# Optimization experiments

Measured on AMD Instinct MI355X. Metric: run time of the kernel, lower is better.

## Reference

```python
import jax, jax.numpy as jnp
import numpy as np

EPS = 1e-5  # torch GroupNorm default eps


def gn(x, g, b):
    # GroupNorm with 1 group on [N, C]: normalize over channel dim per row
    mu = jnp.mean(x, axis=-1, keepdims=True)
    var = jnp.var(x, axis=-1, keepdims=True)
    return (x - mu) * jax.lax.rsqrt(var + EPS) * g + b


def setup_inputs() -> dict:
    N, A, E, D = 500000, 20000, 500000, 128
    key = jax.random.key(0)
    ks = jax.random.split(key, 12)
    s = 0.05
    return {
        "map_x": jax.random.normal(ks[0], (N, 8), jnp.float32),
        "agt_x": jax.random.normal(ks[1], (A, 80), jnp.float32),
        "u": jax.random.randint(ks[2], (E,), 0, A),
        "v": jax.random.randint(ks[3], (E,), 0, N),
        # map_fc: Linear(8,D) with bias, then custom Linear(D,D,bias=False)+GN+ReLU
        "W0": jax.random.normal(ks[4], (D, 8), jnp.float32) * s,
        "b0": jnp.zeros((D,), jnp.float32),
        "W1": jax.random.normal(ks[5], (D, D), jnp.float32) * s,
        "g1": jnp.ones((D,), jnp.float32),
        "b1": jnp.zeros((D,), jnp.float32),
        # agt_fc: Linear(80, D, bias=False)
        "Wa": jax.random.normal(ks[6], (D, 80), jnp.float32) * s,
        # self.bn GroupNorm params
        "g_bn": jnp.ones((D,), jnp.float32),
        "b_bn": jnp.zeros((D,), jnp.float32),
        # self.fc: Linear(2D, D, bias=False)+GN+ReLU
        "Wf": jax.random.normal(ks[7], (D, 2 * D), jnp.float32) * s,
        "g_fc": jnp.ones((D,), jnp.float32),
        "b_fc": jnp.zeros((D,), jnp.float32),
    }


def reference(map_x, agt_x, u, v, W0, b0, W1, g1, b1, Wa, g_bn, b_bn, Wf, g_fc, b_fc):
    # map_fc: Linear+ReLU, then Linear(no bias)+GN+ReLU
    h = jax.nn.relu(map_x @ W0.T + b0)                      # [N, D]
    h = jax.nn.relu(gn(h @ W1.T, g1, b1))                   # [N, D]
    # agent messages: project agents once (A < E), then gather per edge
    msg = (agt_x @ Wa.T)[u]                                 # [E, D]
    tmp = jnp.zeros_like(h).at[v].add(msg)                  # scatter-add into map nodes
    tmp = jax.nn.relu(gn(tmp, g_bn, b_bn))                  # [N, D]
    cat = jnp.concatenate([h, tmp], axis=-1)                # [N, 2D]
    out = jax.nn.relu(gn(cat @ Wf.T, g_fc, b_fc))           # [N, D]
    return out
```

## Files before the change

### kernel.cpp

```cpp
#include <hip/hip_runtime.h>
#include <stdint.h>

#define EPS 1e-5f

typedef short bh8 __attribute__((ext_vector_type(8)));
typedef float f4v __attribute__((ext_vector_type(4)));
typedef unsigned short ushort_t;

static __device__ __forceinline__ unsigned short f2bf(float f) {
    unsigned u = __builtin_bit_cast(unsigned, f);
    u += 0x7fffu + ((u >> 16) & 1u);
    return (unsigned short)(u >> 16);
}

static __device__ __forceinline__ float bfbits(unsigned x) {
    return __builtin_bit_cast(float, x);
}

static __device__ __forceinline__ void acc16(float* tv, uint4 qa, uint4 qb) {
    unsigned wd[8] = {qa.x, qa.y, qa.z, qa.w, qb.x, qb.y, qb.z, qb.w};
#pragma unroll
    for (int p = 0; p < 8; ++p) {
        tv[2 * p + 0] += bfbits(wd[p] << 16);
        tv[2 * p + 1] += bfbits(wd[p] & 0xffff0000u);
    }
}


__global__ __launch_bounds__(256) void prep(const float* __restrict__ W1,
                                            const float* __restrict__ Wf,
                                            ushort_t* __restrict__ W1b,
                                            ushort_t* __restrict__ Wfb,
                                            int* __restrict__ cnt, int n) {
    int i = blockIdx.x * 256 + threadIdx.x;
    if (i < 16384) W1b[i] = f2bf(W1[i]);
    else if (i < 49152) { int j = i - 16384; Wfb[j] = f2bf(Wf[j]); }
    for (int k = i; k < n; k += gridDim.x * 256) cnt[k] = 0;
}

__global__ __launch_bounds__(256) void proj_agents(const float* __restrict__ agt,
                                                   const float* __restrict__ Wa,
                                                   unsigned short* __restrict__ Pb) {
    __shared__ float WT[80 * 128];
    __shared__ float xT[80][32];
    int t = threadIdx.x;
    int row0 = blockIdx.x * 32;
#pragma unroll
    for (int m = 0; m < 40; ++m) {
        int f = t + 256 * m;
        int k = f >> 7, c = f & 127;
        WT[f] = Wa[c * 80 + k];
    }
#pragma unroll
    for (int m = 0; m < 10; ++m) {
        int f = t + 256 * m;
        int r = f / 80, k = f - r * 80;
        xT[k][r] = agt[(size_t)(row0 + r) * 80 + k];
    }
    __syncthreads();
    int tx = t & 31, ty = t >> 5;
    float acc[4][4] = {};
    for (int k = 0; k < 80; ++k) {
        float4 xv = *(const float4*)&xT[k][ty * 4];
        float4 wv = *(const float4*)&WT[k * 128 + tx * 4];
        float xa[4] = {xv.x, xv.y, xv.z, xv.w};
        float wa[4] = {wv.x, wv.y, wv.z, wv.w};
#pragma unroll
        for (int i = 0; i < 4; ++i)
#pragma unroll
            for (int j = 0; j < 4; ++j) acc[i][j] = fmaf(xa[i], wa[j], acc[i][j]);
    }
#pragma unroll
    for (int i = 0; i < 4; ++i) {
        int r = row0 + ty * 4 + i;
        union { unsigned short s[4]; uint2 q; } o;
#pragma unroll
        for (int j = 0; j < 4; ++j) o.s[j] = f2bf(acc[i][j]);
        *(uint2*)&Pb[(size_t)r * 128 + tx * 4] = o.q;
    }
}

__global__ void hist_v(const int* __restrict__ v, int* __restrict__ cnt, int E) {
    int e = blockIdx.x * 256 + threadIdx.x;
    if (e < E) atomicAdd(&cnt[v[e]], 1);
}

__global__ __launch_bounds__(256) void scan1(const int* __restrict__ cnt,
                                             int* __restrict__ rp,
                                             int* __restrict__ partials, int n) {
    __shared__ int lds[256];
    int b = blockIdx.x, t = threadIdx.x;
    int base = b * 4096 + t * 16;
    int vv[16];
    int run = 0;
#pragma unroll
    for (int i = 0; i < 16; ++i) {
        int c = (base + i < n) ? cnt[base + i] : 0;
        vv[i] = run;
        run += c;
    }
    lds[t] = run;
    __syncthreads();
#pragma unroll
    for (int off = 1; off < 256; off <<= 1) {
        int x = (t >= off) ? lds[t - off] : 0;
        __syncthreads();
        lds[t] += x;
        __syncthreads();
    }
    int excl = lds[t] - run;
    if (t == 255) partials[b] = lds[255];
#pragma unroll
    for (int i = 0; i < 16; ++i)
        if (base + i < n) rp[base + i] = excl + vv[i];
}

__global__ __launch_bounds__(256) void scan2(int* __restrict__ partials, int nb) {
    __shared__ int lds[256];
    int t = threadIdx.x;
    int vv = (t < nb) ? partials[t] : 0;
    lds[t] = vv;
    __syncthreads();
#pragma unroll
    for (int off = 1; off < 256; off <<= 1) {
        int x = (t >= off) ? lds[t - off] : 0;
        __syncthreads();
        lds[t] += x;
        __syncthreads();
    }
    if (t < nb) partials[t] = lds[t] - vv;
}

__global__ void scan3(int* __restrict__ rp, const int* __restrict__ partials,
                      int n, int E) {
    int i = blockIdx.x * 256 + threadIdx.x;
    if (i < n) rp[i] += partials[i >> 12];
    if (i == 0) rp[n] = E;
}

__global__ void fill_csr(const int* __restrict__ u, const int* __restrict__ v,
                         const int* __restrict__ rp, int* __restrict__ cnt,
                         int* __restrict__ col, int E) {
    int e = blockIdx.x * 256 + threadIdx.x;
    if (e < E) {
        int vv = v[e];
        int pos = rp[vv] + (atomicSub(&cnt[vv], 1) - 1);
        col[pos] = u[e];
    }
}

__global__ __launch_bounds__(256) void gather_gn(
    const unsigned short* __restrict__ Pb, const int* __restrict__ rp,
    const int* __restrict__ col, const float* __restrict__ g_bn,
    const float* __restrict__ b_bn, ushort_t* __restrict__ catB) {
    const int t = threadIdx.x;
    const int node = blockIdx.x * 32 + (t >> 3);
    const int c0 = (t & 7) * 16;
    const int beg = rp[node];
    const int deg = rp[node + 1] - beg;
    const int ca = col[(deg > 0) ? beg : 0];
    const int cb = col[(deg > 1) ? beg + 1 : 0];
    const int cc = col[(deg > 2) ? beg + 2 : 0];
    const int cd = col[(deg > 3) ? beg + 3 : 0];
    const unsigned short* pB = Pb + c0;
    float tv[16] = {};
    if (deg > 0) { const uint4* p = (const uint4*)(pB + (size_t)ca * 128); acc16(tv, p[0], p[1]); }
    if (deg > 1) { const uint4* p = (const uint4*)(pB + (size_t)cb * 128); acc16(tv, p[0], p[1]); }
    if (deg > 2) { const uint4* p = (const uint4*)(pB + (size_t)cc * 128); acc16(tv, p[0], p[1]); }
    if (deg > 3) { const uint4* p = (const uint4*)(pB + (size_t)cd * 128); acc16(tv, p[0], p[1]); }
    for (int k = 4; k < deg; ++k) {
        const uint4* p = (const uint4*)(pB + (size_t)col[beg + k] * 128);
        acc16(tv, p[0], p[1]);
    }
    float a = 0.f, q = 0.f;
#pragma unroll
    for (int i = 0; i < 16; ++i) { a += tv[i]; q += tv[i] * tv[i]; }
#pragma unroll
    for (int msk = 1; msk < 8; msk <<= 1) {
        a += __shfl_xor(a, msk, 64);
        q += __shfl_xor(q, msk, 64);
    }
    const float mean = a * (1.f / 128.f);
    const float var = q * (1.f / 128.f) - mean * mean;
    const float inv = rsqrtf(var + EPS);
    union { unsigned short s[16]; uint4 q4[2]; } o;
#pragma unroll
    for (int i = 0; i < 16; ++i) {
        const int cch = c0 + i;
        o.s[i] = f2bf(fmaxf((tv[i] - mean) * inv * g_bn[cch] + b_bn[cch], 0.f));
    }
    uint4* dst = (uint4*)(catB + (size_t)node * 128 + c0);
    dst[0] = o.q4[0];
    dst[1] = o.q4[1];
}

__global__ __launch_bounds__(512, 4) void fused(
    const float* __restrict__ mapx, const float* __restrict__ W0,
    const float* __restrict__ b0, const ushort_t* __restrict__ W1b,
    const float* __restrict__ g1, const float* __restrict__ b1,
    const ushort_t* __restrict__ catB, const ushort_t* __restrict__ Wfb,
    const float* __restrict__ g_fc, const float* __restrict__ b_fc,
    float* __restrict__ out, int ntiles)
{
    __shared__ __align__(16) short h0sA[32 * 128], h0sB[32 * 128];
    __shared__ __align__(16) short catsA[32 * 256], catsB[32 * 256];
    __shared__ float W0s[128 * 8];
    __shared__ float b0s[128];
    __shared__ float2 partA[8][32], partB[8][32];
    __shared__ float gA[128], bA[128], gC[128], bC[128];

    const int t = threadIdx.x;
    const int w = t >> 6;
    const int l = t & 63;
    const int l15 = l & 15, lg = l >> 4;

    if (t < 128) {
        gA[t] = g1[t];   bA[t] = b1[t];
        gC[t] = g_fc[t]; bC[t] = b_fc[t];
        b0s[t] = b0[t];
    }
    for (int i = t; i < 1024; i += 512) W0s[i] = W0[i];

    bh8 w1b[4], wfb[8];
    {
        const int wr = 16 * w + l15;
#pragma unroll
        for (int s = 0; s < 4; ++s)
            w1b[s] = *(const bh8*)(W1b + (size_t)wr * 128 + s * 32 + lg * 8);
#pragma unroll
        for (int s = 0; s < 8; ++s)
            wfb[s] = *(const bh8*)(Wfb + (size_t)wr * 256 + s * 32 + lg * 8);
    }
    __syncthreads();

    const f4v fzero = {0.f, 0.f, 0.f, 0.f};
    const int stride = (int)gridDim.x;
    const int npairs = (ntiles + 1) >> 1;

    for (int j = blockIdx.x; j < npairs; j += stride) {
        const int tileA = 2 * j, tileB = 2 * j + 1;
        const bool hasB = (tileB < ntiles);
        const int rowA0 = tileA * 32, rowB0 = tileB * 32;

        {
            const int r = t & 31, cg = t >> 5;
            const int ad = (r * 256 + cg * 16) ^ ((r & 7) << 4);
            {
                float mx[8];
                const float* p = mapx + (size_t)(rowA0 + r) * 8;
                *(float4*)&mx[0] = *(const float4*)p;
                *(float4*)&mx[4] = *(const float4*)(p + 4);
                __align__(16) unsigned short hb[8];
#pragma unroll
                for (int c = 0; c < 8; ++c) {
                    const int cc = 8 * cg + c;
                    float a = b0s[cc];
#pragma unroll
                    for (int jj = 0; jj < 8; ++jj) a = fmaf(mx[jj], W0s[cc * 8 + jj], a);
                    hb[c] = f2bf(fmaxf(a, 0.f));
                }
                *(uint4*)((char*)h0sA + ad) = *(const uint4*)&hb[0];
            }
            if (hasB) {
                float mx[8];
                const float* p = mapx + (size_t)(rowB0 + r) * 8;
                *(float4*)&mx[0] = *(const float4*)p;
                *(float4*)&mx[4] = *(const float4*)(p + 4);
                __align__(16) unsigned short hb[8];
#pragma unroll
                for (int c = 0; c < 8; ++c) {
                    const int cc = 8 * cg + c;
                    float a = b0s[cc];
#pragma unroll
                    for (int jj = 0; jj < 8; ++jj) a = fmaf(mx[jj], W0s[cc * 8 + jj], a);
                    hb[c] = f2bf(fmaxf(a, 0.f));
                }
                *(uint4*)((char*)h0sB + ad) = *(const uint4*)&hb[0];
            }
        }
        {
            const int r2 = t >> 4, cb = (t & 15) * 8;
            const int ad = (r2 * 512 + 256 + cb * 2) ^ ((r2 & 7) << 4);
            uint4 qa = *(const uint4*)(catB + (size_t)(rowA0 + r2) * 128 + cb);
            *(uint4*)((char*)catsA + ad) = qa;
            if (hasB) {
                uint4 qb = *(const uint4*)(catB + (size_t)(rowB0 + r2) * 128 + cb);
                *(uint4*)((char*)catsB + ad) = qb;
            }
        }
        __syncthreads();

        f4v a2A[2], a2B[2];
        a2A[0] = fzero; a2A[1] = fzero; a2B[0] = fzero; a2B[1] = fzero;
#pragma unroll
        for (int s = 0; s < 4; ++s) {
            bh8 afA[2], afB[2];
#pragma unroll
            for (int m = 0; m < 2; ++m) {
                const int row = 16 * m + l15;
                const int a = (row * 256 + s * 64 + lg * 16) ^ ((row & 7) << 4);
                afA[m] = *(const bh8*)((const char*)h0sA + a);
                afB[m] = *(const bh8*)((const char*)h0sB + a);
            }
#pragma unroll
            for (int m = 0; m < 2; ++m) {
                a2A[m] = __builtin_amdgcn_mfma_f32_16x16x32_bf16(w1b[s], afA[m], a2A[m], 0, 0, 0);
                a2B[m] = __builtin_amdgcn_mfma_f32_16x16x32_bf16(w1b[s], afB[m], a2B[m], 0, 0, 0);
            }
        }

#pragma unroll
        for (int m = 0; m < 2; ++m) {
            float aA = a2A[m][0] + a2A[m][1] + a2A[m][2] + a2A[m][3];
            float qA = a2A[m][0] * a2A[m][0] + a2A[m][1] * a2A[m][1] +
                       a2A[m][2] * a2A[m][2] + a2A[m][3] * a2A[m][3];
            float aB = a2B[m][0] + a2B[m][1] + a2B[m][2] + a2B[m][3];
            float qB = a2B[m][0] * a2B[m][0] + a2B[m][1] * a2B[m][1] +
                       a2B[m][2] * a2B[m][2] + a2B[m][3] * a2B[m][3];
            aA += __shfl_xor(aA, 16, 64); qA += __shfl_xor(qA, 16, 64);
            aA += __shfl_xor(aA, 32, 64); qA += __shfl_xor(qA, 32, 64);
            aB += __shfl_xor(aB, 16, 64); qB += __shfl_xor(qB, 16, 64);
            aB += __shfl_xor(aB, 32, 64); qB += __shfl_xor(qB, 32, 64);
            if (lg == 0) {
                partA[w][16 * m + l15] = make_float2(aA, qA);
                partB[w][16 * m + l15] = make_float2(aB, qB);
            }
        }
        __syncthreads();

#pragma unroll
        for (int m = 0; m < 2; ++m) {
            const int row = 16 * m + l15;
            const int c00 = 16 * w + 4 * lg;
            const int ad = (row * 512 + c00 * 2) ^ ((row & 7) << 4);
            {
                float a = 0.f, q = 0.f;
#pragma unroll
                for (int pw = 0; pw < 8; ++pw) {
                    float2 pq = partA[pw][row];
                    a += pq.x; q += pq.y;
                }
                const float mean = a * (1.f / 128.f);
                const float var = q * (1.f / 128.f) - mean * mean;
                const float inv = rsqrtf(var + EPS);
                union { unsigned short s[4]; uint2 q2; } o;
#pragma unroll
                for (int reg = 0; reg < 4; ++reg) {
                    float v2 = (a2A[m][reg] - mean) * inv * gA[c00 + reg] + bA[c00 + reg];
                    o.s[reg] = f2bf(fmaxf(v2, 0.f));
                }
                *(uint2*)((char*)catsA + ad) = o.q2;
            }
            {
                float a = 0.f, q = 0.f;
#pragma unroll
                for (int pw = 0; pw < 8; ++pw) {
                    float2 pq = partB[pw][row];
                    a += pq.x; q += pq.y;
                }
                const float mean = a * (1.f / 128.f);
                const float var = q * (1.f / 128.f) - mean * mean;
                const float inv = rsqrtf(var + EPS);
                union { unsigned short s[4]; uint2 q2; } o;
#pragma unroll
                for (int reg = 0; reg < 4; ++reg) {
                    float v2 = (a2B[m][reg] - mean) * inv * gA[c00 + reg] + bA[c00 + reg];
                    o.s[reg] = f2bf(fmaxf(v2, 0.f));
                }
                *(uint2*)((char*)catsB + ad) = o.q2;
            }
        }
        __syncthreads();

        f4v a3A[2], a3B[2];
        a3A[0] = fzero; a3A[1] = fzero; a3B[0] = fzero; a3B[1] = fzero;
#pragma unroll
        for (int s = 0; s < 8; ++s) {
            bh8 afA[2], afB[2];
#pragma unroll
            for (int m = 0; m < 2; ++m) {
                const int row = 16 * m + l15;
                const int a = (row * 512 + s * 64 + lg * 16) ^ ((row & 7) << 4);
                afA[m] = *(const bh8*)((const char*)catsA + a);
                afB[m] = *(const bh8*)((const char*)catsB + a);
            }
#pragma unroll
            for (int m = 0; m < 2; ++m) {
                a3A[m] = __builtin_amdgcn_mfma_f32_16x16x32_bf16(wfb[s], afA[m], a3A[m], 0, 0, 0);
                a3B[m] = __builtin_amdgcn_mfma_f32_16x16x32_bf16(wfb[s], afB[m], a3B[m], 0, 0, 0);
            }
        }

#pragma unroll
        for (int m = 0; m < 2; ++m) {
            float aA = a3A[m][0] + a3A[m][1] + a3A[m][2] + a3A[m][3];
            float qA = a3A[m][0] * a3A[m][0] + a3A[m][1] * a3A[m][1] +
                       a3A[m][2] * a3A[m][2] + a3A[m][3] * a3A[m][3];
            float aB = a3B[m][0] + a3B[m][1] + a3B[m][2] + a3B[m][3];
            float qB = a3B[m][0] * a3B[m][0] + a3B[m][1] * a3B[m][1] +
                       a3B[m][2] * a3B[m][2] + a3B[m][3] * a3B[m][3];
            aA += __shfl_xor(aA, 16, 64); qA += __shfl_xor(qA, 16, 64);
            aA += __shfl_xor(aA, 32, 64); qA += __shfl_xor(qA, 32, 64);
            aB += __shfl_xor(aB, 16, 64); qB += __shfl_xor(qB, 16, 64);
            aB += __shfl_xor(aB, 32, 64); qB += __shfl_xor(qB, 32, 64);
            if (lg == 0) {
                partA[w][16 * m + l15] = make_float2(aA, qA);
                partB[w][16 * m + l15] = make_float2(aB, qB);
            }
        }
        __syncthreads();

#pragma unroll
        for (int m = 0; m < 2; ++m) {
            const int row = 16 * m + l15;
            const int c00 = 16 * w + 4 * lg;
            {
                float a = 0.f, q = 0.f;
#pragma unroll
                for (int pw = 0; pw < 8; ++pw) {
                    float2 pq = partA[pw][row];
                    a += pq.x; q += pq.y;
                }
                const float mean = a * (1.f / 128.f);
                const float var = q * (1.f / 128.f) - mean * mean;
                const float inv = rsqrtf(var + EPS);
                float4 o;
                o.x = fmaxf((a3A[m][0] - mean) * inv * gC[c00 + 0] + bC[c00 + 0], 0.f);
                o.y = fmaxf((a3A[m][1] - mean) * inv * gC[c00 + 1] + bC[c00 + 1], 0.f);
                o.z = fmaxf((a3A[m][2] - mean) * inv * gC[c00 + 2] + bC[c00 + 2], 0.f);
                o.w = fmaxf((a3A[m][3] - mean) * inv * gC[c00 + 3] + bC[c00 + 3], 0.f);
                *(float4*)&out[(size_t)(rowA0 + row) * 128 + c00] = o;
            }
            if (hasB) {
                float a = 0.f, q = 0.f;
#pragma unroll
                for (int pw = 0; pw < 8; ++pw) {
                    float2 pq = partB[pw][row];
                    a += pq.x; q += pq.y;
                }
                const float mean = a * (1.f / 128.f);
                const float var = q * (1.f / 128.f) - mean * mean;
                const float inv = rsqrtf(var + EPS);
                float4 o;
                o.x = fmaxf((a3B[m][0] - mean) * inv * gC[c00 + 0] + bC[c00 + 0], 0.f);
                o.y = fmaxf((a3B[m][1] - mean) * inv * gC[c00 + 1] + bC[c00 + 1], 0.f);
                o.z = fmaxf((a3B[m][2] - mean) * inv * gC[c00 + 2] + bC[c00 + 2], 0.f);
                o.w = fmaxf((a3B[m][3] - mean) * inv * gC[c00 + 3] + bC[c00 + 3], 0.f);
                *(float4*)&out[(size_t)(rowB0 + row) * 128 + c00] = o;
            }
        }
    }
}

extern "C" void kernel_launch(void* const* d_in, const int* in_sizes, int n_in,
                              void* d_out, int out_size, void* d_ws, size_t ws_size,
                              hipStream_t stream) {
    const float* mapx = (const float*)d_in[0];
    const float* agt  = (const float*)d_in[1];
    const int*   u    = (const int*)d_in[2];
    const int*   v    = (const int*)d_in[3];
    const float* W0   = (const float*)d_in[4];
    const float* b0   = (const float*)d_in[5];
    const float* W1   = (const float*)d_in[6];
    const float* g1   = (const float*)d_in[7];
    const float* b1   = (const float*)d_in[8];
    const float* Wa   = (const float*)d_in[9];
    const float* g_bn = (const float*)d_in[10];
    const float* b_bn = (const float*)d_in[11];
    const float* Wf   = (const float*)d_in[12];
    const float* g_fc = (const float*)d_in[13];
    const float* b_fc = (const float*)d_in[14];
    int N = in_sizes[0] / 8;
    int A = in_sizes[1] / 80;
    int E = in_sizes[2];
    float* out = (float*)d_out;

    char* ws = (char*)d_ws;
    unsigned short* Pb  = (unsigned short*)(ws + 0);
    ushort_t* W1b       = (ushort_t*)(ws + 5160960);
    ushort_t* Wfb       = (ushort_t*)(ws + 5193728);
    int*      cnt       = (int*)(ws + 5259264);
    int*      rp        = (int*)(ws + 9259264);
    int*      partials  = (int*)(ws + 11259392);
    int*      colv      = (int*)(ws + 11261440);
    ushort_t* catB      = (ushort_t*)(ws + 16777216);

    const int nb_scan = (N + 4095) / 4096;
    const int nb_e = (E + 255) / 256;

    prep<<<512, 256, 0, stream>>>(W1, Wf, W1b, Wfb, cnt, N);
    hist_v<<<nb_e, 256, 0, stream>>>(v, cnt, E);
    proj_agents<<<A / 32, 256, 0, stream>>>(agt, Wa, Pb);
    scan1<<<nb_scan, 256, 0, stream>>>(cnt, rp, partials, N);
    scan2<<<1, 256, 0, stream>>>(partials, nb_scan);
    scan3<<<(N + 255) / 256, 256, 0, stream>>>(rp, partials, N, E);
    fill_csr<<<nb_e, 256, 0, stream>>>(u, v, rp, cnt, colv, E);
    gather_gn<<<N / 32, 256, 0, stream>>>(Pb, rp, colv, g_bn, b_bn, catB);

    int ntiles = N / 32;
    fused<<<512, 512, 0, stream>>>(mapx, W0, b0, W1b, g1, b1, catB,
                                   Wfb, g_fc, b_fc, out, ntiles);
}
```

Baseline: 352.9 us.

## Shrink fused kernel LDS by reusing h0 buffers, merge scan2 into scan3

```diff
diff --git a/kernel.cpp b/kernel.cpp
--- a/kernel.cpp
+++ b/kernel.cpp
@@ -115,26 +115,19 @@
         if (base + i < n) rp[base + i] = excl + vv[i];
 }
 
-__global__ __launch_bounds__(256) void scan2(int* __restrict__ partials, int nb) {
-    __shared__ int lds[256];
-    int t = threadIdx.x;
-    int vv = (t < nb) ? partials[t] : 0;
-    lds[t] = vv;
+__global__ __launch_bounds__(256) void scan3(int* __restrict__ rp,
+                                             const int* __restrict__ partials,
+                                             int n, int E, int nb) {
+    __shared__ int pref;
+    int i = blockIdx.x * 256 + threadIdx.x;
+    int chunk = (blockIdx.x * 256) >> 12;
+    if (threadIdx.x == 0) {
+        int s = 0;
+        for (int b = 0; b < chunk; ++b) s += partials[b];
+        pref = s;
+    }
     __syncthreads();
-#pragma unroll
-    for (int off = 1; off < 256; off <<= 1) {
-        int x = (t >= off) ? lds[t - off] : 0;
-        __syncthreads();
-        lds[t] += x;
-        __syncthreads();
-    }
-    if (t < nb) partials[t] = lds[t] - vv;
-}
-
-__global__ void scan3(int* __restrict__ rp, const int* __restrict__ partials,
-                      int n, int E) {
-    int i = blockIdx.x * 256 + threadIdx.x;
-    if (i < n) rp[i] += partials[i >> 12];
+    if (i < n) rp[i] += pref;
     if (i == 0) rp[n] = E;
 }
 
@@ -203,7 +196,7 @@
     float* __restrict__ out, int ntiles)
 {
     __shared__ __align__(16) short h0sA[32 * 128], h0sB[32 * 128];
-    __shared__ __align__(16) short catsA[32 * 256], catsB[32 * 256];
+    __shared__ __align__(16) short msgA[32 * 128], msgB[32 * 128];
     __shared__ float W0s[128 * 8];
     __shared__ float b0s[128];
     __shared__ float2 partA[8][32], partB[8][32];
@@ -279,13 +272,13 @@
             }
         }
         {
-            const int r2 = t >> 4, cb = (t & 15) * 8;
-            const int ad = (r2 * 512 + 256 + cb * 2) ^ ((r2 & 7) << 4);
-            uint4 qa = *(const uint4*)(catB + (size_t)(rowA0 + r2) * 128 + cb);
-            *(uint4*)((char*)catsA + ad) = qa;
+            const int r2 = t >> 4, cb = (t & 15) * 16;
+            const int ad = (r2 * 256 + cb) ^ ((r2 & 7) << 4);
+            uint4 qa = *(const uint4*)((const char*)(catB + (size_t)(rowA0 + r2) * 128) + cb);
+            *(uint4*)((char*)msgA + ad) = qa;
             if (hasB) {
-                uint4 qb = *(const uint4*)(catB + (size_t)(rowB0 + r2) * 128 + cb);
-                *(uint4*)((char*)catsB + ad) = qb;
+                uint4 qb = *(const uint4*)((const char*)(catB + (size_t)(rowB0 + r2) * 128) + cb);
+                *(uint4*)((char*)msgB + ad) = qb;
             }
         }
         __syncthreads();
@@ -332,7 +325,7 @@
         for (int m = 0; m < 2; ++m) {
             const int row = 16 * m + l15;
             const int c00 = 16 * w + 4 * lg;
-            const int ad = (row * 512 + c00 * 2) ^ ((row & 7) << 4);
+            const int ad = (row * 256 + c00 * 2) ^ ((row & 7) << 4);
             {
                 float a = 0.f, q = 0.f;
 #pragma unroll
@@ -349,7 +342,7 @@
                     float v2 = (a2A[m][reg] - mean) * inv * gA[c00 + reg] + bA[c00 + reg];
                     o.s[reg] = f2bf(fmaxf(v2, 0.f));
                 }
-                *(uint2*)((char*)catsA + ad) = o.q2;
+                *(uint2*)((char*)h0sA + ad) = o.q2;
             }
             {
                 float a = 0.f, q = 0.f;
@@ -367,7 +360,7 @@
                     float v2 = (a2B[m][reg] - mean) * inv * gA[c00 + reg] + bA[c00 + reg];
                     o.s[reg] = f2bf(fmaxf(v2, 0.f));
                 }
-                *(uint2*)((char*)catsB + ad) = o.q2;
+                *(uint2*)((char*)h0sB + ad) = o.q2;
             }
         }
         __syncthreads();
@@ -375,19 +368,35 @@
         f4v a3A[2], a3B[2];
         a3A[0] = fzero; a3A[1] = fzero; a3B[0] = fzero; a3B[1] = fzero;
 #pragma unroll
-        for (int s = 0; s < 8; ++s) {
+        for (int s = 0; s < 4; ++s) {
             bh8 afA[2], afB[2];
 #pragma unroll
             for (int m = 0; m < 2; ++m) {
                 const int row = 16 * m + l15;
-                const int a = (row * 512 + s * 64 + lg * 16) ^ ((row & 7) << 4);
-                afA[m] = *(const bh8*)((const char*)catsA + a);
-                afB[m] = *(const bh8*)((const char*)catsB + a);
+                const int a = (row * 256 + s * 64 + lg * 16) ^ ((row & 7) << 4);
+                afA[m] = *(const bh8*)((const char*)h0sA + a);
+                afB[m] = *(const bh8*)((const char*)h0sB + a);
             }
 #pragma unroll
             for (int m = 0; m < 2; ++m) {
                 a3A[m] = __builtin_amdgcn_mfma_f32_16x16x32_bf16(wfb[s], afA[m], a3A[m], 0, 0, 0);
                 a3B[m] = __builtin_amdgcn_mfma_f32_16x16x32_bf16(wfb[s], afB[m], a3B[m], 0, 0, 0);
+            }
+        }
+#pragma unroll
+        for (int s = 0; s < 4; ++s) {
+            bh8 afA[2], afB[2];
+#pragma unroll
+            for (int m = 0; m < 2; ++m) {
+                const int row = 16 * m + l15;
+                const int a = (row * 256 + s * 64 + lg * 16) ^ ((row & 7) << 4);
+                afA[m] = *(const bh8*)((const char*)msgA + a);
+                afB[m] = *(const bh8*)((const char*)msgB + a);
+            }
+#pragma unroll
+            for (int m = 0; m < 2; ++m) {
+                a3A[m] = __builtin_amdgcn_mfma_f32_16x16x32_bf16(wfb[4 + s], afA[m], a3A[m], 0, 0, 0);
+                a3B[m] = __builtin_amdgcn_mfma_f32_16x16x32_bf16(wfb[4 + s], afB[m], a3B[m], 0, 0, 0);
             }
         }
 
@@ -492,12 +501,11 @@
     hist_v<<<nb_e, 256, 0, stream>>>(v, cnt, E);
     proj_agents<<<A / 32, 256, 0, stream>>>(agt, Wa, Pb);
     scan1<<<nb_scan, 256, 0, stream>>>(cnt, rp, partials, N);
-    scan2<<<1, 256, 0, stream>>>(partials, nb_scan);
-    scan3<<<(N + 255) / 256, 256, 0, stream>>>(rp, partials, N, E);
+    scan3<<<(N + 255) / 256, 256, 0, stream>>>(rp, partials, N, E, nb_scan);
     fill_csr<<<nb_e, 256, 0, stream>>>(u, v, rp, cnt, colv, E);
     gather_gn<<<N / 32, 256, 0, stream>>>(Pb, rp, colv, g_bn, b_bn, catB);
 
     int ntiles = N / 32;
-    fused<<<512, 512, 0, stream>>>(mapx, W0, b0, W1b, g1, b1, catB,
+    fused<<<768, 512, 0, stream>>>(mapx, W0, b0, W1b, g1, b1, catB,
                                    Wfb, g_fc, b_fc, out, ntiles);
 }
```

Result: faster. 329.9 us (-6.5%).
